# Kernel optimization log

Hardware: AMD Instinct MI355X
Metric: run time of the kernel (lower is better)

Reference implementation:

```python
import jax, jax.numpy as jnp
import numpy as np

N = 50000          # total nodes
E = 800000         # edges (avg degree 16)
IN = 128           # in_feat
HID = 64           # hidden per head
HEADS = (4, 4, 1)
NEG_SLOPE = 0.2    # DGL GATConv leaky_relu default


def setup_inputs() -> dict:
    key = jax.random.key(0)
    ks = jax.random.split(key, 16)

    def w(k, shape, fan_in):
        return jax.random.normal(k, shape, jnp.float32) / np.float32(np.sqrt(fan_in))

    inp = {
        "feat": jax.random.normal(ks[0], (N, IN), jnp.float32),
        "src": jax.random.randint(ks[1], (E,), 0, N, jnp.int32),
        "dst": jax.random.randint(ks[2], (E,), 0, N, jnp.int32),
    }
    dims = [(IN, HEADS[0]), (HID * HEADS[0], HEADS[1]), (HID * HEADS[1], HEADS[2])]
    j = 3
    for i, (din, h) in enumerate(dims, 1):
        inp[f"W{i}"] = w(ks[j], (din, h * HID), din); j += 1
        inp[f"al{i}"] = w(ks[j], (h, HID), HID); j += 1
        inp[f"ar{i}"] = w(ks[j], (h, HID), HID); j += 1
        inp[f"b{i}"] = jnp.zeros((h * HID,), jnp.float32)
    return inp


def gat_layer(x, W, al, ar, b, src, dst, n_heads):
    # DGL GATConv: linear -> per-node attn logits -> edge leaky_relu ->
    # per-dst segment softmax -> weighted scatter-sum -> + bias
    h = (x @ W).reshape(N, n_heads, HID)                     # [N,H,D]
    el = jnp.einsum("nhd,hd->nh", h, al)                     # [N,H]
    er = jnp.einsum("nhd,hd->nh", h, ar)                     # [N,H]
    e = jax.nn.leaky_relu(el[src] + er[dst], NEG_SLOPE)      # [E,H]
    m = jax.ops.segment_max(e, dst, num_segments=N)          # [N,H]
    m = jnp.where(jnp.isfinite(m), m, 0.0)                   # empty segments -> -inf
    ex = jnp.exp(e - m[dst])                                 # [E,H]
    s = jax.ops.segment_sum(ex, dst, num_segments=N)         # [N,H]
    alpha = ex / s[dst]                                      # [E,H]
    msg = h[src] * alpha[:, :, None]                         # [E,H,D]
    out = jax.ops.segment_sum(msg, dst, num_segments=N)      # [N,H,D]
    return out + b.reshape(1, n_heads, HID)


def reference(feat, src, dst, W1, al1, ar1, b1, W2, al2, ar2, b2, W3, al3, ar3, b3):
    h = jax.nn.elu(gat_layer(feat, W1, al1, ar1, b1, src, dst, HEADS[0]))
    h = h.reshape(N, HEADS[0] * HID)                         # flatten heads
    h = jax.nn.elu(gat_layer(h, W2, al2, ar2, b2, src, dst, HEADS[1]))
    h = h.reshape(N, HEADS[1] * HID)
    h = gat_layer(h, W3, al3, ar3, b3, src, dst, HEADS[2])   # no activation
    return h.mean(axis=1)                                    # [N, HID]
```

## Files before the change

### kernel.cpp

```cpp
#include <hip/hip_runtime.h>
#include <math.h>

#define HID 64
#define NSLOPE 0.2f
#define SB 512

typedef __attribute__((ext_vector_type(8))) short short8v;
typedef __attribute__((ext_vector_type(4))) float float4v;

__device__ inline unsigned short f2bf(float x) {
  unsigned u = __float_as_uint(x);
  u += 0x7fffu + ((u >> 16) & 1u);
  return (unsigned short)(u >> 16);
}
__device__ inline float bf2f(unsigned short h) {
  return __uint_as_float(((unsigned)h) << 16);
}

__global__ __launch_bounds__(256) void k_split(const float* __restrict__ x,
    unsigned short* __restrict__ hi, unsigned short* __restrict__ lo, int n) {
  int i = blockIdx.x * 256 + threadIdx.x;
  if (i < n) {
    float v = x[i];
    unsigned short h = f2bf(v);
    hi[i] = h;
    lo[i] = f2bf(v - bf2f(h));
  }
}

__global__ __launch_bounds__(256) void k_wsplit(const float* __restrict__ W,
    unsigned short* __restrict__ Whi, unsigned short* __restrict__ Wlo, int K, int N) {
  int i = blockIdx.x * 256 + threadIdx.x;
  if (i < N * K) {
    int n = i / K, k = i - n * K;
    float v = W[(size_t)k * N + n];
    unsigned short h = f2bf(v);
    Whi[i] = h;
    Wlo[i] = f2bf(v - bf2f(h));
  }
}

__global__ __launch_bounds__(256) void gemm_split(
    const unsigned short* __restrict__ Ahi, const unsigned short* __restrict__ Alo,
    const unsigned short* __restrict__ Bhi, const unsigned short* __restrict__ Blo,
    float* __restrict__ C, int M, int Nc, int K) {
  __shared__ __align__(16) unsigned short AsHi[128 * 40];
  __shared__ __align__(16) unsigned short AsLo[128 * 40];
  __shared__ __align__(16) unsigned short BsHi[128 * 40];
  __shared__ __align__(16) unsigned short BsLo[128 * 40];
  const int tid = threadIdx.x;
  const int lane = tid & 63, wid = tid >> 6;
  const int wr = wid >> 1, wc = wid & 1;
  const int row0 = blockIdx.y * 128;
  const int col0 = blockIdx.x * 128;
  float4v acc[4][4];
  #pragma unroll
  for (int mi = 0; mi < 4; ++mi)
    #pragma unroll
    for (int ni = 0; ni < 4; ++ni)
      acc[mi][ni] = (float4v){0.f, 0.f, 0.f, 0.f};

  const int sr = tid >> 2;
  const int sc8 = (tid & 3) * 8;
  const int lr = lane & 15, lk = (lane >> 4) * 8;

  for (int k0 = 0; k0 < K; k0 += 32) {
    #pragma unroll
    for (int half = 0; half < 2; ++half) {
      int row = sr + half * 64;
      int arow = row0 + row; if (arow > M - 1) arow = M - 1;
      int brow = col0 + row; if (brow > Nc - 1) brow = Nc - 1;
      *(short8v*)&AsHi[row * 40 + sc8] = *(const short8v*)&Ahi[(size_t)arow * K + k0 + sc8];
      *(short8v*)&AsLo[row * 40 + sc8] = *(const short8v*)&Alo[(size_t)arow * K + k0 + sc8];
      *(short8v*)&BsHi[row * 40 + sc8] = *(const short8v*)&Bhi[(size_t)brow * K + k0 + sc8];
      *(short8v*)&BsLo[row * 40 + sc8] = *(const short8v*)&Blo[(size_t)brow * K + k0 + sc8];
    }
    __syncthreads();
    short8v ah[4], alv[4], bh[4], bl[4];
    #pragma unroll
    for (int mi = 0; mi < 4; ++mi) {
      int r = wr * 64 + mi * 16 + lr;
      ah[mi]  = *(const short8v*)&AsHi[r * 40 + lk];
      alv[mi] = *(const short8v*)&AsLo[r * 40 + lk];
    }
    #pragma unroll
    for (int ni = 0; ni < 4; ++ni) {
      int r = wc * 64 + ni * 16 + lr;
      bh[ni] = *(const short8v*)&BsHi[r * 40 + lk];
      bl[ni] = *(const short8v*)&BsLo[r * 40 + lk];
    }
    #pragma unroll
    for (int mi = 0; mi < 4; ++mi)
      #pragma unroll
      for (int ni = 0; ni < 4; ++ni) {
        acc[mi][ni] = __builtin_amdgcn_mfma_f32_16x16x32_bf16(ah[mi], bh[ni], acc[mi][ni], 0, 0, 0);
        acc[mi][ni] = __builtin_amdgcn_mfma_f32_16x16x32_bf16(ah[mi], bl[ni], acc[mi][ni], 0, 0, 0);
        acc[mi][ni] = __builtin_amdgcn_mfma_f32_16x16x32_bf16(alv[mi], bh[ni], acc[mi][ni], 0, 0, 0);
      }
    __syncthreads();
  }
  #pragma unroll
  for (int mi = 0; mi < 4; ++mi) {
    int rbase = row0 + wr * 64 + mi * 16 + (lane >> 4) * 4;
    #pragma unroll
    for (int ni = 0; ni < 4; ++ni) {
      int cc = col0 + wc * 64 + ni * 16 + (lane & 15);
      if (cc < Nc) {
        #pragma unroll
        for (int q = 0; q < 4; ++q) {
          int rr = rbase + q;
          if (rr < M) C[(size_t)rr * Nc + cc] = acc[mi][ni][q];
        }
      }
    }
  }
}

__global__ __launch_bounds__(64) void elr_kernel(const float* __restrict__ h,
    const float* __restrict__ al, const float* __restrict__ ar,
    float* __restrict__ el, float* __restrict__ er, int H) {
  int n = blockIdx.x, lane = threadIdx.x;
  const float* hr = h + (size_t)n * H * HID;
  for (int hh = 0; hh < H; ++hh) {
    float v = hr[hh * HID + lane];
    float a = v * al[hh * HID + lane];
    float b = v * ar[hh * HID + lane];
    #pragma unroll
    for (int o = 32; o > 0; o >>= 1) { a += __shfl_xor(a, o); b += __shfl_xor(b, o); }
    if (lane == 0) { el[n * H + hh] = a; er[n * H + hh] = b; }
  }
}

__global__ void k_count(const int* __restrict__ dst, int* __restrict__ deg, int E) {
  int e = blockIdx.x * blockDim.x + threadIdx.x;
  if (e < E) atomicAdd(&deg[dst[e]], 1);
}
__global__ __launch_bounds__(SB) void k_blocksums(const int* __restrict__ deg,
                                                  int* __restrict__ bsums, int n) {
  __shared__ int s[SB];
  int t = threadIdx.x, i = blockIdx.x * SB + t;
  s[t] = (i < n) ? deg[i] : 0;
  __syncthreads();
  for (int o = SB >> 1; o > 0; o >>= 1) { if (t < o) s[t] += s[t + o]; __syncthreads(); }
  if (t == 0) bsums[blockIdx.x] = s[0];
}
__global__ __launch_bounds__(SB) void k_scancarry(const int* __restrict__ bsums,
                                                   int* __restrict__ carry, int nb) {
  __shared__ int s[SB];
  int t = threadIdx.x;
  int v = (t < nb) ? bsums[t] : 0;
  s[t] = v; __syncthreads();
  for (int o = 1; o < SB; o <<= 1) {
    int u = (t >= o) ? s[t - o] : 0;
    __syncthreads(); s[t] += u; __syncthreads();
  }
  if (t < nb) carry[t] = s[t] - v;
}
__global__ __launch_bounds__(SB) void k_offsets(const int* __restrict__ deg,
    const int* __restrict__ carry, int* __restrict__ offs, int n, int E) {
  __shared__ int s[SB];
  int t = threadIdx.x, i = blockIdx.x * SB + t;
  int v = (i < n) ? deg[i] : 0;
  s[t] = v; __syncthreads();
  for (int o = 1; o < SB; o <<= 1) {
    int u = (t >= o) ? s[t - o] : 0;
    __syncthreads(); s[t] += u; __syncthreads();
  }
  if (i < n) offs[i] = carry[blockIdx.x] + s[t] - v;
  if (i == n) offs[n] = E;
}
__global__ void k_fill(const int* __restrict__ src, const int* __restrict__ dst,
                       const int* __restrict__ offs, int* __restrict__ cursor,
                       int* __restrict__ esrc, int E) {
  int e = blockIdx.x * blockDim.x + threadIdx.x;
  if (e < E) {
    int d = dst[e];
    int slot = offs[d] + atomicAdd(&cursor[d], 1);
    esrc[slot] = src[e];
  }
}

template<int H, bool DO_ELU, bool SPLITOUT>
__global__ __launch_bounds__(64) void agg_kernel(const float* __restrict__ hbuf,
    const float* __restrict__ el, const float* __restrict__ er,
    const int* __restrict__ offs, const int* __restrict__ esrc,
    const float* __restrict__ bias,
    unsigned short* __restrict__ outHi, unsigned short* __restrict__ outLo,
    float* __restrict__ outF) {
  const int n = blockIdx.x, lane = threadIdx.x;
  const int off = offs[n];
  const int deg = offs[n + 1] - off;
  float erh[H], mh[H], sh[H], inv[H], acc[H];
  #pragma unroll
  for (int hh = 0; hh < H; ++hh) {
    erh[hh] = er[n * H + hh]; mh[hh] = -1e30f; sh[hh] = 0.f; acc[hh] = 0.f;
  }
  for (int base = 0; base < deg; base += 64) {
    int i = base + lane;
    float eh[H];
    if (i < deg) {
      int s = esrc[off + i];
      #pragma unroll
      for (int hh = 0; hh < H; ++hh) {
        float e = el[s * H + hh] + erh[hh];
        eh[hh] = e > 0.f ? e : NSLOPE * e;
      }
    } else {
      #pragma unroll
      for (int hh = 0; hh < H; ++hh) eh[hh] = -1e30f;
    }
    #pragma unroll
    for (int hh = 0; hh < H; ++hh) {
      float v = eh[hh];
      #pragma unroll
      for (int o = 32; o > 0; o >>= 1) v = fmaxf(v, __shfl_xor(v, o));
      mh[hh] = fmaxf(mh[hh], v);
    }
  }
  auto compute_ex = [&](int i, float (&t)[H]) {
    if (i < deg) {
      int s = esrc[off + i];
      #pragma unroll
      for (int hh = 0; hh < H; ++hh) {
        float e = el[s * H + hh] + erh[hh];
        e = e > 0.f ? e : NSLOPE * e;
        t[hh] = __expf(e - mh[hh]);
      }
    } else {
      #pragma unroll
      for (int hh = 0; hh < H; ++hh) t[hh] = 0.f;
    }
  };
  float ex0[H], ex1[H], ex2[H], ex3[H];
  compute_ex(lane, ex0);
  compute_ex(64 + lane, ex1);
  compute_ex(128 + lane, ex2);
  compute_ex(192 + lane, ex3);
  #pragma unroll
  for (int hh = 0; hh < H; ++hh) sh[hh] = ex0[hh] + ex1[hh] + ex2[hh] + ex3[hh];
  for (int base = 256; base < deg; base += 64) {
    float t[H]; compute_ex(base + lane, t);
    #pragma unroll
    for (int hh = 0; hh < H; ++hh) sh[hh] += t[hh];
  }
  #pragma unroll
  for (int hh = 0; hh < H; ++hh) {
    float v = sh[hh];
    #pragma unroll
    for (int o = 32; o > 0; o >>= 1) v += __shfl_xor(v, o);
    inv[hh] = v > 0.f ? 1.f / v : 0.f;
  }
  auto pv = [&](int cbase, const float (&exv)[H]) {
    int lim = deg - cbase; lim = lim > 64 ? 64 : lim;
    int t = 0;
    for (; t + 4 <= lim; t += 4) {
      int s0 = esrc[off + cbase + t + 0];
      int s1 = esrc[off + cbase + t + 1];
      int s2 = esrc[off + cbase + t + 2];
      int s3 = esrc[off + cbase + t + 3];
      const float* p0 = hbuf + (size_t)s0 * (H * HID);
      const float* p1 = hbuf + (size_t)s1 * (H * HID);
      const float* p2 = hbuf + (size_t)s2 * (H * HID);
      const float* p3 = hbuf + (size_t)s3 * (H * HID);
      #pragma unroll
      for (int hh = 0; hh < H; ++hh) {
        float a0 = __shfl(exv[hh], t + 0) * inv[hh];
        float a1 = __shfl(exv[hh], t + 1) * inv[hh];
        float a2 = __shfl(exv[hh], t + 2) * inv[hh];
        float a3 = __shfl(exv[hh], t + 3) * inv[hh];
        float v0 = p0[hh * HID + lane], v1 = p1[hh * HID + lane];
        float v2 = p2[hh * HID + lane], v3 = p3[hh * HID + lane];
        acc[hh] = fmaf(v0, a0, acc[hh]);
        acc[hh] = fmaf(v1, a1, acc[hh]);
        acc[hh] = fmaf(v2, a2, acc[hh]);
        acc[hh] = fmaf(v3, a3, acc[hh]);
      }
    }
    for (; t < lim; ++t) {
      int s = esrc[off + cbase + t];
      const float* hp = hbuf + (size_t)s * (H * HID);
      #pragma unroll
      for (int hh = 0; hh < H; ++hh) {
        float a = __shfl(exv[hh], t) * inv[hh];
        acc[hh] = fmaf(hp[hh * HID + lane], a, acc[hh]);
      }
    }
  };
  if (deg > 0)   pv(0, ex0);
  if (deg > 64)  pv(64, ex1);
  if (deg > 128) pv(128, ex2);
  if (deg > 192) pv(192, ex3);
  for (int i = 256; i < deg; ++i) {
    int s = esrc[off + i];
    const float* hp = hbuf + (size_t)s * (H * HID);
    #pragma unroll
    for (int hh = 0; hh < H; ++hh) {
      float e = el[s * H + hh] + erh[hh];
      e = e > 0.f ? e : NSLOPE * e;
      float a = __expf(e - mh[hh]) * inv[hh];
      acc[hh] = fmaf(hp[hh * HID + lane], a, acc[hh]);
    }
  }
  #pragma unroll
  for (int hh = 0; hh < H; ++hh) {
    float v = acc[hh] + bias[hh * HID + lane];
    if (DO_ELU) v = v > 0.f ? v : expm1f(v);
    size_t oi = (size_t)n * (H * HID) + hh * HID + lane;
    if (SPLITOUT) {
      unsigned short hb = f2bf(v);
      outHi[oi] = hb;
      outLo[oi] = f2bf(v - bf2f(hb));
    } else {
      outF[oi] = v;
    }
  }
}

extern "C" void kernel_launch(void* const* d_in, const int* in_sizes, int n_in,
                              void* d_out, int out_size, void* d_ws, size_t ws_size,
                              hipStream_t stream) {
  const float* feat = (const float*)d_in[0];
  const int* src = (const int*)d_in[1];
  const int* dst = (const int*)d_in[2];
  const float* W1 = (const float*)d_in[3];
  const float* al1 = (const float*)d_in[4];
  const float* ar1 = (const float*)d_in[5];
  const float* b1 = (const float*)d_in[6];
  const float* W2 = (const float*)d_in[7];
  const float* al2 = (const float*)d_in[8];
  const float* ar2 = (const float*)d_in[9];
  const float* b2 = (const float*)d_in[10];
  const float* W3 = (const float*)d_in[11];
  const float* al3 = (const float*)d_in[12];
  const float* ar3 = (const float*)d_in[13];
  const float* b3 = (const float*)d_in[14];
  const int N = in_sizes[0] / 128;
  const int E = in_sizes[1];

  char* w = (char*)d_ws;
  auto alloc = [&](size_t bytes) {
    void* p = (void*)w;
    w += (bytes + 255) & ~(size_t)255;
    return p;
  };
  unsigned short* pHi = (unsigned short*)alloc((size_t)N * 256 * 2);
  unsigned short* pLo = (unsigned short*)alloc((size_t)N * 256 * 2);
  float* Cbuf = (float*)alloc((size_t)N * 256 * 4);
  float* el = (float*)alloc((size_t)N * 4 * 4);
  float* er = (float*)alloc((size_t)N * 4 * 4);
  int* deg = (int*)alloc((size_t)N * 4);
  int* cursor = (int*)alloc((size_t)N * 4);
  int* offs = (int*)alloc((size_t)(N + 1) * 4);
  int nb = (N + SB - 1) / SB;
  int* bsums = (int*)alloc((size_t)nb * 4);
  int* carry = (int*)alloc((size_t)nb * 4);
  int* esrc = (int*)alloc((size_t)E * 4);
  unsigned short* W1h = (unsigned short*)alloc((size_t)256 * 128 * 2);
  unsigned short* W1l = (unsigned short*)alloc((size_t)256 * 128 * 2);
  unsigned short* W2h = (unsigned short*)alloc((size_t)256 * 256 * 2);
  unsigned short* W2l = (unsigned short*)alloc((size_t)256 * 256 * 2);
  unsigned short* W3h = (unsigned short*)alloc((size_t)64 * 256 * 2);
  unsigned short* W3l = (unsigned short*)alloc((size_t)64 * 256 * 2);

  hipMemsetAsync(deg, 0, (size_t)N * 4, stream);
  hipMemsetAsync(cursor, 0, (size_t)N * 4, stream);
  int eb = (E + 255) / 256;
  k_count<<<eb, 256, 0, stream>>>(dst, deg, E);
  k_blocksums<<<nb, SB, 0, stream>>>(deg, bsums, N);
  k_scancarry<<<1, SB, 0, stream>>>(bsums, carry, nb);
  k_offsets<<<nb, SB, 0, stream>>>(deg, carry, offs, N, E);
  k_fill<<<eb, 256, 0, stream>>>(src, dst, offs, cursor, esrc, E);

  k_wsplit<<<(256 * 128 + 255) / 256, 256, 0, stream>>>(W1, W1h, W1l, 128, 256);
  k_wsplit<<<(256 * 256 + 255) / 256, 256, 0, stream>>>(W2, W2h, W2l, 256, 256);
  k_wsplit<<<(64 * 256 + 255) / 256, 256, 0, stream>>>(W3, W3h, W3l, 256, 64);

  k_split<<<((N * 128) + 255) / 256, 256, 0, stream>>>(feat, pHi, pLo, N * 128);

  int rg = (N + 127) / 128;
  gemm_split<<<dim3(2, rg), 256, 0, stream>>>(pHi, pLo, W1h, W1l, Cbuf, N, 256, 128);
  elr_kernel<<<N, 64, 0, stream>>>(Cbuf, al1, ar1, el, er, 4);
  agg_kernel<4, true, true><<<N, 64, 0, stream>>>(Cbuf, el, er, offs, esrc, b1, pHi, pLo, nullptr);
  gemm_split<<<dim3(2, rg), 256, 0, stream>>>(pHi, pLo, W2h, W2l, Cbuf, N, 256, 256);
  elr_kernel<<<N, 64, 0, stream>>>(Cbuf, al2, ar2, el, er, 4);
  agg_kernel<4, true, true><<<N, 64, 0, stream>>>(Cbuf, el, er, offs, esrc, b2, pHi, pLo, nullptr);
  gemm_split<<<dim3(1, rg), 256, 0, stream>>>(pHi, pLo, W3h, W3l, Cbuf, N, 64, 256);
  elr_kernel<<<N, 64, 0, stream>>>(Cbuf, al3, ar3, el, er, 1);
  agg_kernel<1, false, false><<<N, 64, 0, stream>>>(Cbuf, el, er, offs, esrc, b3, nullptr, nullptr, (float*)d_out);
}
```

Before: 545.2 us.

## Gather bf16 head-interleaved features in aggregation instead of fp32 rows

The GEMM epilogue now also writes a bf16 copy of the projected features with heads interleaved per lane, so each lane loads one 8-byte uint2 holding all four heads of its column. The aggregation kernel gathers from this compact buffer, halving gather bytes, and unrolls the edge loop to 8 outstanding loads. The softmax normalisation is folded into the exp values ahead of the loop. This adds an extra store pass in the GEMM and lowers feature precision in the message sum to bf16, which may hurt accuracy.

```diff
diff --git a/kernel.cpp b/kernel.cpp
--- a/kernel.cpp
+++ b/kernel.cpp
@@ -16,6 +16,8 @@
 __device__ inline float bf2f(unsigned short h) {
   return __uint_as_float(((unsigned)h) << 16);
 }
+__device__ inline float bflo(unsigned u) { return __uint_as_float(u << 16); }
+__device__ inline float bfhi(unsigned u) { return __uint_as_float(u & 0xffff0000u); }
 
 __global__ __launch_bounds__(256) void k_split(const float* __restrict__ x,
     unsigned short* __restrict__ hi, unsigned short* __restrict__ lo, int n) {
@@ -43,7 +45,7 @@
 __global__ __launch_bounds__(256) void gemm_split(
     const unsigned short* __restrict__ Ahi, const unsigned short* __restrict__ Alo,
     const unsigned short* __restrict__ Bhi, const unsigned short* __restrict__ Blo,
-    float* __restrict__ C, int M, int Nc, int K) {
+    float* __restrict__ C, unsigned short* __restrict__ Gp, int M, int Nc, int K, int H) {
   __shared__ __align__(16) unsigned short AsHi[128 * 40];
   __shared__ __align__(16) unsigned short AsLo[128 * 40];
   __shared__ __align__(16) unsigned short BsHi[128 * 40];
@@ -106,10 +108,15 @@
     for (int ni = 0; ni < 4; ++ni) {
       int cc = col0 + wc * 64 + ni * 16 + (lane & 15);
       if (cc < Nc) {
+        int gcol = (cc & 63) * H + (cc >> 6);
         #pragma unroll
         for (int q = 0; q < 4; ++q) {
           int rr = rbase + q;
-          if (rr < M) C[(size_t)rr * Nc + cc] = acc[mi][ni][q];
+          if (rr < M) {
+            float v = acc[mi][ni][q];
+            C[(size_t)rr * Nc + cc] = v;
+            Gp[(size_t)rr * Nc + gcol] = f2bf(v);
+          }
         }
       }
     }
@@ -181,7 +188,7 @@
 }
 
 template<int H, bool DO_ELU, bool SPLITOUT>
-__global__ __launch_bounds__(64) void agg_kernel(const float* __restrict__ hbuf,
+__global__ __launch_bounds__(64) void agg_kernel(const unsigned short* __restrict__ gp,
     const float* __restrict__ el, const float* __restrict__ er,
     const int* __restrict__ offs, const int* __restrict__ esrc,
     const float* __restrict__ bias,
@@ -250,39 +257,48 @@
     for (int o = 32; o > 0; o >>= 1) v += __shfl_xor(v, o);
     inv[hh] = v > 0.f ? 1.f / v : 0.f;
   }
+  #pragma unroll
+  for (int hh = 0; hh < H; ++hh) {
+    ex0[hh] *= inv[hh]; ex1[hh] *= inv[hh]; ex2[hh] *= inv[hh]; ex3[hh] *= inv[hh];
+  }
   auto pv = [&](int cbase, const float (&exv)[H]) {
     int lim = deg - cbase; lim = lim > 64 ? 64 : lim;
     int t = 0;
-    for (; t + 4 <= lim; t += 4) {
-      int s0 = esrc[off + cbase + t + 0];
-      int s1 = esrc[off + cbase + t + 1];
-      int s2 = esrc[off + cbase + t + 2];
-      int s3 = esrc[off + cbase + t + 3];
-      const float* p0 = hbuf + (size_t)s0 * (H * HID);
-      const float* p1 = hbuf + (size_t)s1 * (H * HID);
-      const float* p2 = hbuf + (size_t)s2 * (H * HID);
-      const float* p3 = hbuf + (size_t)s3 * (H * HID);
-      #pragma unroll
-      for (int hh = 0; hh < H; ++hh) {
-        float a0 = __shfl(exv[hh], t + 0) * inv[hh];
-        float a1 = __shfl(exv[hh], t + 1) * inv[hh];
-        float a2 = __shfl(exv[hh], t + 2) * inv[hh];
-        float a3 = __shfl(exv[hh], t + 3) * inv[hh];
-        float v0 = p0[hh * HID + lane], v1 = p1[hh * HID + lane];
-        float v2 = p2[hh * HID + lane], v3 = p3[hh * HID + lane];
-        acc[hh] = fmaf(v0, a0, acc[hh]);
-        acc[hh] = fmaf(v1, a1, acc[hh]);
-        acc[hh] = fmaf(v2, a2, acc[hh]);
-        acc[hh] = fmaf(v3, a3, acc[hh]);
+    for (; t + 8 <= lim; t += 8) {
+      int s[8];
+      #pragma unroll
+      for (int j = 0; j < 8; ++j) s[j] = esrc[off + cbase + t + j];
+      if (H == 4) {
+        uint2 g[8];
+        #pragma unroll
+        for (int j = 0; j < 8; ++j)
+          g[j] = *(const uint2*)&gp[(size_t)s[j] * 256 + lane * 4];
+        #pragma unroll
+        for (int j = 0; j < 8; ++j) {
+          acc[0] = fmaf(bflo(g[j].x), __shfl(exv[0], t + j), acc[0]);
+          acc[1] = fmaf(bfhi(g[j].x), __shfl(exv[1], t + j), acc[1]);
+          acc[2] = fmaf(bflo(g[j].y), __shfl(exv[2], t + j), acc[2]);
+          acc[3] = fmaf(bfhi(g[j].y), __shfl(exv[3], t + j), acc[3]);
+        }
+      } else {
+        unsigned short g[8];
+        #pragma unroll
+        for (int j = 0; j < 8; ++j) g[j] = gp[(size_t)s[j] * 64 + lane];
+        #pragma unroll
+        for (int j = 0; j < 8; ++j)
+          acc[0] = fmaf(bf2f(g[j]), __shfl(exv[0], t + j), acc[0]);
       }
     }
     for (; t < lim; ++t) {
       int s = esrc[off + cbase + t];
-      const float* hp = hbuf + (size_t)s * (H * HID);
-      #pragma unroll
-      for (int hh = 0; hh < H; ++hh) {
-        float a = __shfl(exv[hh], t) * inv[hh];
-        acc[hh] = fmaf(hp[hh * HID + lane], a, acc[hh]);
+      if (H == 4) {
+        uint2 g = *(const uint2*)&gp[(size_t)s * 256 + lane * 4];
+        acc[0] = fmaf(bflo(g.x), __shfl(exv[0], t), acc[0]);
+        acc[1] = fmaf(bfhi(g.x), __shfl(exv[1], t), acc[1]);
+        acc[2] = fmaf(bflo(g.y), __shfl(exv[2], t), acc[2]);
+        acc[3] = fmaf(bfhi(g.y), __shfl(exv[3], t), acc[3]);
+      } else {
+        acc[0] = fmaf(bf2f(gp[(size_t)s * 64 + lane]), __shfl(exv[0], t), acc[0]);
       }
     }
   };
@@ -292,13 +308,14 @@
   if (deg > 192) pv(192, ex3);
   for (int i = 256; i < deg; ++i) {
     int s = esrc[off + i];
-    const float* hp = hbuf + (size_t)s * (H * HID);
     #pragma unroll
     for (int hh = 0; hh < H; ++hh) {
       float e = el[s * H + hh] + erh[hh];
       e = e > 0.f ? e : NSLOPE * e;
       float a = __expf(e - mh[hh]) * inv[hh];
-      acc[hh] = fmaf(hp[hh * HID + lane], a, acc[hh]);
+      float v = (H == 4) ? bf2f(gp[(size_t)s * 256 + lane * 4 + hh])
+                         : bf2f(gp[(size_t)s * 64 + lane]);
+      acc[hh] = fmaf(v, a, acc[hh]);
     }
   }
   #pragma unroll
@@ -346,6 +363,7 @@
   unsigned short* pHi = (unsigned short*)alloc((size_t)N * 256 * 2);
   unsigned short* pLo = (unsigned short*)alloc((size_t)N * 256 * 2);
   float* Cbuf = (float*)alloc((size_t)N * 256 * 4);
+  unsigned short* Gp = (unsigned short*)alloc((size_t)N * 256 * 2);
   float* el = (float*)alloc((size_t)N * 4 * 4);
   float* er = (float*)alloc((size_t)N * 4 * 4);
   int* deg = (int*)alloc((size_t)N * 4);
@@ -378,13 +396,13 @@
   k_split<<<((N * 128) + 255) / 256, 256, 0, stream>>>(feat, pHi, pLo, N * 128);
 
   int rg = (N + 127) / 128;
-  gemm_split<<<dim3(2, rg), 256, 0, stream>>>(pHi, pLo, W1h, W1l, Cbuf, N, 256, 128);
+  gemm_split<<<dim3(2, rg), 256, 0, stream>>>(pHi, pLo, W1h, W1l, Cbuf, Gp, N, 256, 128, 4);
   elr_kernel<<<N, 64, 0, stream>>>(Cbuf, al1, ar1, el, er, 4);
-  agg_kernel<4, true, true><<<N, 64, 0, stream>>>(Cbuf, el, er, offs, esrc, b1, pHi, pLo, nullptr);
-  gemm_split<<<dim3(2, rg), 256, 0, stream>>>(pHi, pLo, W2h, W2l, Cbuf, N, 256, 256);
+  agg_kernel<4, true, true><<<N, 64, 0, stream>>>(Gp, el, er, offs, esrc, b1, pHi, pLo, nullptr);
+  gemm_split<<<dim3(2, rg), 256, 0, stream>>>(pHi, pLo, W2h, W2l, Cbuf, Gp, N, 256, 256, 4);
   elr_kernel<<<N, 64, 0, stream>>>(Cbuf, al2, ar2, el, er, 4);
-  agg_kernel<4, true, true><<<N, 64, 0, stream>>>(Cbuf, el, er, offs, esrc, b2, pHi, pLo, nullptr);
-  gemm_split<<<dim3(1, rg), 256, 0, stream>>>(pHi, pLo, W3h, W3l, Cbuf, N, 64, 256);
+  agg_kernel<4, true, true><<<N, 64, 0, stream>>>(Gp, el, er, offs, esrc, b2, pHi, pLo, nullptr);
+  gemm_split<<<dim3(1, rg), 256, 0, stream>>>(pHi, pLo, W3h, W3l, Cbuf, Gp, N, 64, 256, 1);
   elr_kernel<<<N, 64, 0, stream>>>(Cbuf, al3, ar3, el, er, 1);
-  agg_kernel<1, false, false><<<N, 64, 0, stream>>>(Cbuf, el, er, offs, esrc, b3, nullptr, nullptr, (float*)d_out);
-}
+  agg_kernel<1, false, false><<<N, 64, 0, stream>>>(Gp, el, er, offs, esrc, b3, nullptr, nullptr, (float*)d_out);
+}
```

Result: faster. 508.2 us (-6.8%).
